# Performance work log

Hardware: AMD Instinct MI355X
Metric: run time of the kernel (lower is better)

The kernel has to match this reference:

```python
import jax, jax.numpy as jnp
import numpy as np

N, K, C, ECTX, HID = 4096, 48, 128, 384, 512
EPS = 1e-5
SCALE = 30.0

def _gelu(x):
    return jax.nn.gelu(x, approximate=False)

def _layernorm(x, g, b):
    mu = jnp.mean(x, axis=-1, keepdims=True)
    var = jnp.var(x, axis=-1, keepdims=True)
    return (x - mu) * jax.lax.rsqrt(var + EPS) * g + b

def setup_inputs() -> dict:
    key = jax.random.key(0)
    ks = jax.random.split(key, 12)
    d_in = C + ECTX  # 512
    def lin(k, out, inp):
        kw, kb = jax.random.split(k)
        lim = 1.0 / np.sqrt(inp)
        W = jax.random.uniform(kw, (out, inp), jnp.float32, -lim, lim)
        b = jax.random.uniform(kb, (out,), jnp.float32, -lim, lim)
        return W, b
    W_m1, b_m1 = lin(ks[0], C, d_in)   # message MLP: in->width
    W_m2, b_m2 = lin(ks[1], C, C)      # width->width
    W_m3, b_m3 = lin(ks[2], C, C)      # width->out
    W_d1, b_d1 = lin(ks[3], HID, C)    # dense MLP: in->hidden
    W_d2, b_d2 = lin(ks[4], C, HID)    # hidden->out
    return {
        "node_features": jax.random.normal(ks[5], (N, C), jnp.float32),
        "layer_edge_features": jax.random.normal(ks[6], (N, K, ECTX), jnp.float32),
        "mask": jnp.ones((N,), jnp.float32),
        "attention_mask": jnp.ones((N, K), jnp.float32),
        "W_m1": W_m1, "b_m1": b_m1, "W_m2": W_m2, "b_m2": b_m2,
        "W_m3": W_m3, "b_m3": b_m3,
        "g1": jnp.ones((C,), jnp.float32), "beta1": jnp.zeros((C,), jnp.float32),
        "W_d1": W_d1, "b_d1": b_d1, "W_d2": W_d2, "b_d2": b_d2,
        "g2": jnp.ones((C,), jnp.float32), "beta2": jnp.zeros((C,), jnp.float32),
    }

def reference(node_features, layer_edge_features, mask, attention_mask,
              W_m1, b_m1, W_m2, b_m2, W_m3, b_m3, g1, beta1,
              W_d1, b_d1, W_d2, b_d2, g2, beta2):
    # broadcast node features to every neighbor slot and concat edge context: (N, K, C+ECTX)
    h_exp = jnp.broadcast_to(node_features[:, None, :], (N, K, C))
    mlp_in = jnp.concatenate([h_exp, layer_edge_features], axis=-1)
    # per-edge message MLP (depth=2: two hidden gelu layers, linear out)
    h = _gelu(jnp.einsum("nkd,cd->nkc", mlp_in, W_m1) + b_m1)
    h = _gelu(jnp.einsum("nkc,dc->nkd", h, W_m2) + b_m2)
    message = jnp.einsum("nkc,dc->nkd", h, W_m3) + b_m3
    message = attention_mask[:, :, None] * message
    agg = jnp.sum(message, axis=-2) / SCALE            # (N, C)
    x = node_features + agg
    x = _layernorm(x, g1, beta1)
    # dense MLP (depth=1)
    d = _gelu(jnp.einsum("nc,hc->nh", x, W_d1) + b_d1)
    d = jnp.einsum("nh,ch->nc", d, W_d2) + b_d2
    x = x + d
    x = _layernorm(x, g2, beta2)
    return mask[:, None] * x
```

## Files before the change

kernel.cpp:

```cpp
#include <hip/hip_runtime.h>

#define NN 4096
#define KK 48
#define CC 128
#define EC 384
#define DD 512
#define HH 512

typedef short bf16x8 __attribute__((ext_vector_type(8)));
typedef float f32x4 __attribute__((ext_vector_type(4)));

__device__ __forceinline__ unsigned int pk2(float lo, float hi){
  unsigned int r;
  asm("v_cvt_pk_bf16_f32 %0, %1, %2" : "=v"(r) : "v"(lo), "v"(hi));
  return r;
}
__device__ __forceinline__ unsigned short f2bf(float x){
  return (unsigned short)pk2(x, x);
}
__device__ __forceinline__ bf16x8 pack8(f32x4 a, f32x4 b){
  union { unsigned int w[4]; bf16x8 v; } u;
  u.w[0]=pk2(a[0],a[1]); u.w[1]=pk2(a[2],a[3]);
  u.w[2]=pk2(b[0],b[1]); u.w[3]=pk2(b[2],b[3]);
  return u.v;
}

__device__ __forceinline__ float gelu_f(float x){
  float s = 1.5957691216057308f * (x + 0.044715f*x*x*x);
  float e = __expf(s);
  float t = 1.0f - 2.0f/(e + 1.0f);
  return 0.5f*x*(1.0f + t);
}

__global__ void cvt_kernel(const float* __restrict__ W1, const float* __restrict__ W2,
                           const float* __restrict__ W3, const float* __restrict__ Wd1,
                           const float* __restrict__ Wd2, unsigned short* __restrict__ o){
  int i = blockIdx.x*256 + threadIdx.x;
  float v;
  if      (i <  65536) v = W1[i];
  else if (i <  81920) v = W2[i-65536];
  else if (i <  98304) v = W3[i-81920];
  else if (i < 163840) v = Wd1[i-98304];
  else                 v = Wd2[i-163840];
  o[i] = f2bf(v);
}

__global__ __launch_bounds__(256, 4) void node_kernel(
    const float* __restrict__ nodef, const unsigned short* __restrict__ W1b,
    const float* __restrict__ b1, float* __restrict__ Y)
{
  const int tid  = threadIdx.x;
  const int lane = tid & 63;
  const int wid  = tid >> 6;
  const int l15  = lane & 15;
  const int lg   = lane >> 4;
  const int lg8  = lg*8;
  const int rowb = blockIdx.x*64 + wid*16;

  f32x4 acc[8];
  #pragma unroll
  for (int nt=0; nt<8; ++nt) acc[nt] = (f32x4){0.f,0.f,0.f,0.f};

  const float* arow = nodef + (size_t)(rowb + l15)*CC;
  #pragma unroll
  for (int ks=0; ks<4; ++ks){
    const int k0 = ks*32;
    bf16x8 af = pack8(*(const f32x4*)(arow + k0 + lg8), *(const f32x4*)(arow + k0 + lg8 + 4));
    #pragma unroll
    for (int nt=0; nt<8; ++nt){
      bf16x8 bf_ = *(const bf16x8*)(W1b + (size_t)(nt*16 + l15)*DD + k0 + lg8);
      acc[nt] = __builtin_amdgcn_mfma_f32_16x16x32_bf16(af, bf_, acc[nt], 0,0,0);
    }
  }
  #pragma unroll
  for (int nt=0; nt<8; ++nt){
    const int c = nt*16 + l15;
    const float bb = b1[c];
    #pragma unroll
    for (int j=0; j<4; ++j)
      Y[(size_t)(rowb + lg*4 + j)*CC + c] = acc[nt][j] + bb;
  }
}

__global__ __launch_bounds__(256, 4) void msg_kernel(
    const float* __restrict__ nodef, const float* __restrict__ edgef,
    const float* __restrict__ attn, const float* __restrict__ Y,
    const unsigned short* __restrict__ W1b,
    const unsigned short* __restrict__ W2b, const float* __restrict__ b2,
    const unsigned short* __restrict__ W3b, const float* __restrict__ b3,
    float* __restrict__ x1)
{
  __shared__ __attribute__((aligned(16))) unsigned short H[96][136];

  const int tid  = threadIdx.x;
  const int lane = tid & 63;
  const int wid  = tid >> 6;
  const int wm   = wid & 1;
  const int wn   = wid >> 1;
  const int l15  = lane & 15;
  const int lg   = lane >> 4;
  const int lg8  = lg*8;
  const int node = blockIdx.x*2 + wm;
  const int colb = wn*64;

  const float* erow[3];
  #pragma unroll
  for (int mt=0; mt<3; ++mt)
    erow[mt] = edgef + ((size_t)node*KK + (mt*16 + l15))*EC;

  float yv[4];
  #pragma unroll
  for (int nt=0; nt<4; ++nt)
    yv[nt] = Y[(size_t)node*CC + colb + nt*16 + l15];

  f32x4 acc[3][4];
  #pragma unroll
  for (int mt=0; mt<3; ++mt)
    #pragma unroll
    for (int nt=0; nt<4; ++nt)
      #pragma unroll
      for (int j=0; j<4; ++j) acc[mt][nt][j] = yv[nt];

  bf16x8 aC[3], bC[4], aN[3], bN[4];
  #pragma unroll
  for (int nt=0; nt<4; ++nt)
    bC[nt] = *(const bf16x8*)(W1b + (size_t)(colb + nt*16 + l15)*DD + CC + lg8);
  #pragma unroll
  for (int mt=0; mt<3; ++mt)
    aC[mt] = pack8(*(const f32x4*)(erow[mt] + lg8), *(const f32x4*)(erow[mt] + lg8 + 4));

  #pragma unroll
  for (int ks=0; ks<12; ++ks){
    if (ks < 11){
      const int k1 = (ks+1)*32;
      #pragma unroll
      for (int nt=0; nt<4; ++nt)
        bN[nt] = *(const bf16x8*)(W1b + (size_t)(colb + nt*16 + l15)*DD + CC + k1 + lg8);
      #pragma unroll
      for (int mt=0; mt<3; ++mt)
        aN[mt] = pack8(*(const f32x4*)(erow[mt] + k1 + lg8), *(const f32x4*)(erow[mt] + k1 + lg8 + 4));
    }
    #pragma unroll
    for (int mt=0; mt<3; ++mt)
      #pragma unroll
      for (int nt=0; nt<4; ++nt)
        acc[mt][nt] = __builtin_amdgcn_mfma_f32_16x16x32_bf16(aC[mt], bC[nt], acc[mt][nt], 0,0,0);
    #pragma unroll
    for (int mt=0; mt<3; ++mt) aC[mt] = aN[mt];
    #pragma unroll
    for (int nt=0; nt<4; ++nt) bC[nt] = bN[nt];
  }

  #pragma unroll
  for (int nt=0; nt<4; ++nt){
    const int c = colb + nt*16 + l15;
    #pragma unroll
    for (int mt=0; mt<3; ++mt){
      const int r0 = wm*48 + mt*16 + lg*4;
      #pragma unroll
      for (int j=0; j<4; ++j)
        H[r0+j][c] = f2bf(gelu_f(acc[mt][nt][j]));
    }
  }
  __syncthreads();

  f32x4 a2[3][4];
  #pragma unroll
  for (int mt=0; mt<3; ++mt)
    #pragma unroll
    for (int nt=0; nt<4; ++nt) a2[mt][nt] = (f32x4){0.f,0.f,0.f,0.f};

  #pragma unroll
  for (int ks=0; ks<4; ++ks){
    const int k0 = ks*32;
    bf16x8 bf_[4], af_[3];
    #pragma unroll
    for (int nt=0; nt<4; ++nt)
      bf_[nt] = *(const bf16x8*)(W2b + (size_t)(colb + nt*16 + l15)*CC + k0 + lg8);
    #pragma unroll
    for (int mt=0; mt<3; ++mt)
      af_[mt] = *(const bf16x8*)&H[wm*48 + mt*16 + l15][k0 + lg8];
    #pragma unroll
    for (int mt=0; mt<3; ++mt)
      #pragma unroll
      for (int nt=0; nt<4; ++nt)
        a2[mt][nt] = __builtin_amdgcn_mfma_f32_16x16x32_bf16(af_[mt], bf_[nt], a2[mt][nt], 0,0,0);
  }
  __syncthreads();

  #pragma unroll
  for (int nt=0; nt<4; ++nt){
    const int c = colb + nt*16 + l15;
    const float bb = b2[c];
    #pragma unroll
    for (int mt=0; mt<3; ++mt){
      const int r0 = wm*48 + mt*16 + lg*4;
      #pragma unroll
      for (int j=0; j<4; ++j)
        H[r0+j][c] = f2bf(gelu_f(a2[mt][nt][j] + bb));
    }
  }
  __syncthreads();

  f32x4 a3[3][4];
  #pragma unroll
  for (int mt=0; mt<3; ++mt)
    #pragma unroll
    for (int nt=0; nt<4; ++nt) a3[mt][nt] = (f32x4){0.f,0.f,0.f,0.f};

  #pragma unroll
  for (int ks=0; ks<4; ++ks){
    const int k0 = ks*32;
    bf16x8 bf_[4], af_[3];
    #pragma unroll
    for (int nt=0; nt<4; ++nt)
      bf_[nt] = *(const bf16x8*)(W3b + (size_t)(colb + nt*16 + l15)*CC + k0 + lg8);
    #pragma unroll
    for (int mt=0; mt<3; ++mt)
      af_[mt] = *(const bf16x8*)&H[wm*48 + mt*16 + l15][k0 + lg8];
    #pragma unroll
    for (int mt=0; mt<3; ++mt)
      #pragma unroll
      for (int nt=0; nt<4; ++nt)
        a3[mt][nt] = __builtin_amdgcn_mfma_f32_16x16x32_bf16(af_[mt], bf_[nt], a3[mt][nt], 0,0,0);
  }

  float av[3][4];
  #pragma unroll
  for (int mt=0; mt<3; ++mt)
    #pragma unroll
    for (int j=0; j<4; ++j)
      av[mt][j] = attn[(size_t)node*KK + mt*16 + lg*4 + j];

  #pragma unroll
  for (int nt=0; nt<4; ++nt){
    const int c = colb + nt*16 + l15;
    const float bb = b3[c];
    float t = 0.f;
    #pragma unroll
    for (int mt=0; mt<3; ++mt)
      #pragma unroll
      for (int j=0; j<4; ++j)
        t += (a3[mt][nt][j] + bb) * av[mt][j];
    t += __shfl_xor(t, 16, 64);
    t += __shfl_xor(t, 32, 64);
    if (lg == 0)
      x1[(size_t)node*CC + c] = nodef[(size_t)node*CC + c] + t*(1.0f/30.0f);
  }
}

__global__ __launch_bounds__(256, 2) void post_kernel(
    const float* __restrict__ x1, const float* __restrict__ mask,
    const float* __restrict__ g1, const float* __restrict__ be1,
    const unsigned short* __restrict__ Wd1b, const float* __restrict__ bd1,
    const unsigned short* __restrict__ Wd2b, const float* __restrict__ bd2,
    const float* __restrict__ g2, const float* __restrict__ be2,
    float* __restrict__ out)
{
  __shared__ __attribute__((aligned(16))) unsigned short xlnB[16][136];
  __shared__ __attribute__((aligned(16))) float          xlnF[16][132];
  __shared__ __attribute__((aligned(16))) unsigned short Hb[16][520];
  __shared__ __attribute__((aligned(16))) float          x2s[16][132];

  const int tid  = threadIdx.x;
  const int lane = tid & 63;
  const int wid  = tid >> 6;
  const int l15  = lane & 15;
  const int lg   = lane >> 4;
  const int lg8  = lg*8;
  const int n0   = blockIdx.x * 16;

  {
    const int nl = tid >> 4;
    const int s  = tid & 15;
    const float* row = x1 + (size_t)(n0+nl)*CC + s*8;
    f32x4 a = *(const f32x4*)row;
    f32x4 b = *(const f32x4*)(row+4);
    float sm = (a[0]+a[1])+(a[2]+a[3]) + (b[0]+b[1])+(b[2]+b[3]);
    float sq = a[0]*a[0]+a[1]*a[1]+a[2]*a[2]+a[3]*a[3]
             + b[0]*b[0]+b[1]*b[1]+b[2]*b[2]+b[3]*b[3];
    sm += __shfl_xor(sm,1,64); sq += __shfl_xor(sq,1,64);
    sm += __shfl_xor(sm,2,64); sq += __shfl_xor(sq,2,64);
    sm += __shfl_xor(sm,4,64); sq += __shfl_xor(sq,4,64);
    sm += __shfl_xor(sm,8,64); sq += __shfl_xor(sq,8,64);
    const float mu = sm*(1.f/128.f);
    const float rs = rsqrtf(sq*(1.f/128.f) - mu*mu + 1e-5f);
    #pragma unroll
    for (int j=0; j<8; ++j){
      const int c = s*8+j;
      float xv = (j<4) ? a[j] : b[j-4];
      float y = (xv-mu)*rs*g1[c] + be1[c];
      xlnF[nl][c] = y;
      xlnB[nl][c] = f2bf(y);
    }
  }
  __syncthreads();

  f32x4 a1[8];
  #pragma unroll
  for (int nt=0; nt<8; ++nt) a1[nt] = (f32x4){0.f,0.f,0.f,0.f};
  #pragma unroll
  for (int ks=0; ks<4; ++ks){
    const int k0 = ks*32;
    bf16x8 af = *(const bf16x8*)&xlnB[l15][k0 + lg8];
    #pragma unroll
    for (int nt=0; nt<8; ++nt){
      const int h = wid*128 + nt*16 + l15;
      bf16x8 bf_ = *(const bf16x8*)(Wd1b + (size_t)h*CC + k0 + lg8);
      a1[nt] = __builtin_amdgcn_mfma_f32_16x16x32_bf16(af, bf_, a1[nt], 0,0,0);
    }
  }
  #pragma unroll
  for (int nt=0; nt<8; ++nt){
    const int h = wid*128 + nt*16 + l15;
    const float bb = bd1[h];
    #pragma unroll
    for (int j=0; j<4; ++j)
      Hb[lg*4+j][h] = f2bf(gelu_f(a1[nt][j] + bb));
  }
  __syncthreads();

  f32x4 a2[2];
  #pragma unroll
  for (int nt=0; nt<2; ++nt) a2[nt] = (f32x4){0.f,0.f,0.f,0.f};
  #pragma unroll
  for (int ks=0; ks<16; ++ks){
    const int k0 = ks*32;
    bf16x8 af = *(const bf16x8*)&Hb[l15][k0 + lg8];
    #pragma unroll
    for (int nt=0; nt<2; ++nt){
      const int c = wid*32 + nt*16 + l15;
      bf16x8 bf_ = *(const bf16x8*)(Wd2b + (size_t)c*HH + k0 + lg8);
      a2[nt] = __builtin_amdgcn_mfma_f32_16x16x32_bf16(af, bf_, a2[nt], 0,0,0);
    }
  }
  #pragma unroll
  for (int nt=0; nt<2; ++nt){
    const int c = wid*32 + nt*16 + l15;
    const float bb = bd2[c];
    #pragma unroll
    for (int j=0; j<4; ++j){
      const int r = lg*4 + j;
      x2s[r][c] = xlnF[r][c] + a2[nt][j] + bb;
    }
  }
  __syncthreads();

  {
    const int nl = tid >> 4;
    const int s  = tid & 15;
    float xv[8];
    float sm = 0.f, sq = 0.f;
    #pragma unroll
    for (int j=0; j<8; ++j){ xv[j] = x2s[nl][s*8+j]; sm += xv[j]; sq += xv[j]*xv[j]; }
    sm += __shfl_xor(sm,1,64); sq += __shfl_xor(sq,1,64);
    sm += __shfl_xor(sm,2,64); sq += __shfl_xor(sq,2,64);
    sm += __shfl_xor(sm,4,64); sq += __shfl_xor(sq,4,64);
    sm += __shfl_xor(sm,8,64); sq += __shfl_xor(sq,8,64);
    const float mu = sm*(1.f/128.f);
    const float rs = rsqrtf(sq*(1.f/128.f) - mu*mu + 1e-5f);
    const float mk = mask[n0+nl];
    f32x4 o0, o1;
    #pragma unroll
    for (int j=0; j<8; ++j){
      const int c = s*8+j;
      float y = (xv[j]-mu)*rs*g2[c] + be2[c];
      if (j < 4) o0[j] = mk*y; else o1[j-4] = mk*y;
    }
    float* orow = out + (size_t)(n0+nl)*CC + s*8;
    *(f32x4*)orow     = o0;
    *(f32x4*)(orow+4) = o1;
  }
}

extern "C" void kernel_launch(void* const* d_in, const int* in_sizes, int n_in,
                              void* d_out, int out_size, void* d_ws, size_t ws_size,
                              hipStream_t stream)
{
  (void)in_sizes; (void)n_in; (void)out_size; (void)ws_size;

  const float* nodef = (const float*)d_in[0];
  const float* edgef = (const float*)d_in[1];
  const float* mask  = (const float*)d_in[2];
  const float* attn  = (const float*)d_in[3];
  const float* W_m1  = (const float*)d_in[4];
  const float* b_m1  = (const float*)d_in[5];
  const float* W_m2  = (const float*)d_in[6];
  const float* b_m2  = (const float*)d_in[7];
  const float* W_m3  = (const float*)d_in[8];
  const float* b_m3  = (const float*)d_in[9];
  const float* g1    = (const float*)d_in[10];
  const float* be1   = (const float*)d_in[11];
  const float* W_d1  = (const float*)d_in[12];
  const float* b_d1  = (const float*)d_in[13];
  const float* W_d2  = (const float*)d_in[14];
  const float* b_d2  = (const float*)d_in[15];
  const float* g2    = (const float*)d_in[16];
  const float* be2   = (const float*)d_in[17];

  unsigned short* wsb  = (unsigned short*)d_ws;
  unsigned short* W1b  = wsb;
  unsigned short* W2b  = wsb + 65536;
  unsigned short* W3b  = wsb + 81920;
  unsigned short* Wd1b = wsb + 98304;
  unsigned short* Wd2b = wsb + 163840;
  float* x1 = (float*)((char*)d_ws + 458752);
  float* Y  = (float*)((char*)d_ws + 2555904);

  cvt_kernel<<<896, 256, 0, stream>>>(W_m1, W_m2, W_m3, W_d1, W_d2, wsb);
  node_kernel<<<64, 256, 0, stream>>>(nodef, W1b, b_m1, Y);
  msg_kernel<<<2048, 256, 0, stream>>>(nodef, edgef, attn, Y,
                                       W1b, W2b, b_m2, W3b, b_m3, x1);
  post_kernel<<<256, 256, 0, stream>>>(x1, mask, g1, be1, Wd1b, b_d1,
                                       Wd2b, b_d2, g2, be2, (float*)d_out);
}
```

Measured before the change: 544.9 us.

## Fuse post-MLP into message kernel and stage edge features via async LDS DMA

Edge-feature tiles for the first message layer now go through a triple-buffered LDS ring filled by global_load_lds with an XOR swizzle, instead of direct per-lane global loads. The post kernel (layernorm, dense MLP, layernorm, mask) is folded into the tail of msg_kernel, so the x1 round trip and one launch go away. Occupancy drops from 4 to 2 blocks per SM because of the larger LDS footprint. The fused dense MLP uses only 2 of 16 MFMA rows per block, which wastes matrix throughput and re-reads the dense weights once per block.

```diff
diff --git a/kernel.cpp b/kernel.cpp
--- a/kernel.cpp
+++ b/kernel.cpp
@@ -9,27 +9,27 @@
 
 typedef short bf16x8 __attribute__((ext_vector_type(8)));
 typedef float f32x4 __attribute__((ext_vector_type(4)));
-
-__device__ __forceinline__ unsigned int pk2(float lo, float hi){
-  unsigned int r;
-  asm("v_cvt_pk_bf16_f32 %0, %1, %2" : "=v"(r) : "v"(lo), "v"(hi));
-  return r;
-}
-__device__ __forceinline__ unsigned short f2bf(float x){
-  return (unsigned short)pk2(x, x);
-}
+typedef unsigned int u32;
+
+typedef const __attribute__((address_space(1))) void* gas1_t;
+typedef __attribute__((address_space(3))) void* las3_t;
+
+#define CB() asm volatile("" ::: "memory")
+
+__device__ __forceinline__ u32 pk2(float lo, float hi){
+  u32 r; asm("v_cvt_pk_bf16_f32 %0, %1, %2" : "=v"(r) : "v"(lo), "v"(hi)); return r;
+}
+__device__ __forceinline__ unsigned short f2bf(float x){ return (unsigned short)pk2(x,x); }
 __device__ __forceinline__ bf16x8 pack8(f32x4 a, f32x4 b){
-  union { unsigned int w[4]; bf16x8 v; } u;
+  union { u32 w[4]; bf16x8 v; } u;
   u.w[0]=pk2(a[0],a[1]); u.w[1]=pk2(a[2],a[3]);
   u.w[2]=pk2(b[0],b[1]); u.w[3]=pk2(b[2],b[3]);
   return u.v;
 }
-
 __device__ __forceinline__ float gelu_f(float x){
-  float s = 1.5957691216057308f * (x + 0.044715f*x*x*x);
+  float s = 1.5957691216057308f*(x + 0.044715f*x*x*x);
   float e = __expf(s);
-  float t = 1.0f - 2.0f/(e + 1.0f);
-  return 0.5f*x*(1.0f + t);
+  return 0.5f*x*(1.f + (1.f - 2.f/(e+1.f)));
 }
 
 __global__ void cvt_kernel(const float* __restrict__ W1, const float* __restrict__ W2,
@@ -82,15 +82,27 @@
   }
 }
 
-__global__ __launch_bounds__(256, 4) void msg_kernel(
+__global__ __launch_bounds__(256, 2) void msg_kernel(
     const float* __restrict__ nodef, const float* __restrict__ edgef,
     const float* __restrict__ attn, const float* __restrict__ Y,
     const unsigned short* __restrict__ W1b,
     const unsigned short* __restrict__ W2b, const float* __restrict__ b2,
     const unsigned short* __restrict__ W3b, const float* __restrict__ b3,
-    float* __restrict__ x1)
+    const float* __restrict__ g1v, const float* __restrict__ be1,
+    const unsigned short* __restrict__ Wd1b, const float* __restrict__ bd1,
+    const unsigned short* __restrict__ Wd2b, const float* __restrict__ bd2,
+    const float* __restrict__ g2v, const float* __restrict__ be2,
+    const float* __restrict__ maskv, float* __restrict__ out)
 {
+  __shared__ __attribute__((aligned(16))) char SA[36864];
   __shared__ __attribute__((aligned(16))) unsigned short H[96][136];
+
+  float (*Abuf)[96*32] = (float(*)[96*32])SA;
+  unsigned short (*xlnB)[136] = (unsigned short(*)[136])SA;
+  float* xlnF = (float*)(SA + 4352);
+  float* x1s  = (float*)(SA + 5376);
+  unsigned short (*Hd)[520] = (unsigned short(*)[520])(SA + 6400);
+  float* x2s  = (float*)(SA + 23040);
 
   const int tid  = threadIdx.x;
   const int lane = tid & 63;
@@ -100,13 +112,28 @@
   const int l15  = lane & 15;
   const int lg   = lane >> 4;
   const int lg8  = lg*8;
-  const int node = blockIdx.x*2 + wm;
-  const int colb = wn*64;
-
-  const float* erow[3];
-  #pragma unroll
-  for (int mt=0; mt<3; ++mt)
-    erow[mt] = edgef + ((size_t)node*KK + (mt*16 + l15))*EC;
+  const int node0 = blockIdx.x*2;
+  const int node  = node0 + wm;
+  const int colb  = wn*64;
+
+  const float* gsrc = edgef + (size_t)node0*KK*EC;
+  int dma_r[3], dma_s4[3];
+  #pragma unroll
+  for (int i=0;i<3;++i){
+    int c = wid*3 + i;
+    int r = c*8 + (lane>>3);
+    int s = (lane&7) ^ (r&7);
+    dma_r[i] = r;
+    dma_s4[i] = s*4;
+  }
+
+#define STAGE(B_, T_)                                                              \
+  { _Pragma("unroll")                                                              \
+    for (int i_=0;i_<3;++i_){                                                      \
+      __builtin_amdgcn_global_load_lds(                                            \
+        (gas1_t)(gsrc + (size_t)dma_r[i_]*EC + (T_)*32 + dma_s4[i_]),              \
+        (las3_t)&Abuf[B_][(wid*3+i_)*256], 16, 0, 0);                              \
+    } }
 
   float yv[4];
   #pragma unroll
@@ -121,32 +148,45 @@
       #pragma unroll
       for (int j=0; j<4; ++j) acc[mt][nt][j] = yv[nt];
 
-  bf16x8 aC[3], bC[4], aN[3], bN[4];
+  CB();
+  bf16x8 bC[4], bN[4];
   #pragma unroll
   for (int nt=0; nt<4; ++nt)
     bC[nt] = *(const bf16x8*)(W1b + (size_t)(colb + nt*16 + l15)*DD + CC + lg8);
-  #pragma unroll
-  for (int mt=0; mt<3; ++mt)
-    aC[mt] = pack8(*(const f32x4*)(erow[mt] + lg8), *(const f32x4*)(erow[mt] + lg8 + 4));
-
-  #pragma unroll
-  for (int ks=0; ks<12; ++ks){
-    if (ks < 11){
-      const int k1 = (ks+1)*32;
+  CB();
+  STAGE(0, 0); CB();
+  STAGE(1, 1); CB();
+
+  #pragma unroll
+  for (int t=0; t<12; ++t){
+    const int cur = t % 3;
+    if (t < 11){
       #pragma unroll
       for (int nt=0; nt<4; ++nt)
-        bN[nt] = *(const bf16x8*)(W1b + (size_t)(colb + nt*16 + l15)*DD + CC + k1 + lg8);
-      #pragma unroll
-      for (int mt=0; mt<3; ++mt)
-        aN[mt] = pack8(*(const f32x4*)(erow[mt] + k1 + lg8), *(const f32x4*)(erow[mt] + k1 + lg8 + 4));
+        bN[nt] = *(const bf16x8*)(W1b + (size_t)(colb + nt*16 + l15)*DD + CC + (t+1)*32 + lg8);
+    }
+    CB();
+    if (t < 11) asm volatile("s_waitcnt vmcnt(7)" ::: "memory");
+    else        asm volatile("s_waitcnt vmcnt(0)" ::: "memory");
+    __builtin_amdgcn_s_barrier();
+    CB();
+    if (t+2 < 12){ STAGE((t+2)%3, t+2); }
+    CB();
+    bf16x8 a_[3];
+    #pragma unroll
+    for (int mt=0; mt<3; ++mt){
+      const int r  = wm*48 + mt*16 + l15;
+      const int s0 = (2*lg)   ^ (r&7);
+      const int s1 = (2*lg+1) ^ (r&7);
+      f32x4 lo = *(const f32x4*)&Abuf[cur][r*32 + s0*4];
+      f32x4 hi = *(const f32x4*)&Abuf[cur][r*32 + s1*4];
+      a_[mt] = pack8(lo, hi);
     }
     #pragma unroll
     for (int mt=0; mt<3; ++mt)
       #pragma unroll
       for (int nt=0; nt<4; ++nt)
-        acc[mt][nt] = __builtin_amdgcn_mfma_f32_16x16x32_bf16(aC[mt], bC[nt], acc[mt][nt], 0,0,0);
-    #pragma unroll
-    for (int mt=0; mt<3; ++mt) aC[mt] = aN[mt];
+        acc[mt][nt] = __builtin_amdgcn_mfma_f32_16x16x32_bf16(a_[mt], bC[nt], acc[mt][nt], 0,0,0);
     #pragma unroll
     for (int nt=0; nt<4; ++nt) bC[nt] = bN[nt];
   }
@@ -232,6 +272,7 @@
     for (int j=0; j<4; ++j)
       av[mt][j] = attn[(size_t)node*KK + mt*16 + lg*4 + j];
 
+  float tt[4];
   #pragma unroll
   for (int nt=0; nt<4; ++nt){
     const int c = colb + nt*16 + l15;
@@ -244,61 +285,37 @@
         t += (a3[mt][nt][j] + bb) * av[mt][j];
     t += __shfl_xor(t, 16, 64);
     t += __shfl_xor(t, 32, 64);
-    if (lg == 0)
-      x1[(size_t)node*CC + c] = nodef[(size_t)node*CC + c] + t*(1.0f/30.0f);
-  }
-}
-
-__global__ __launch_bounds__(256, 2) void post_kernel(
-    const float* __restrict__ x1, const float* __restrict__ mask,
-    const float* __restrict__ g1, const float* __restrict__ be1,
-    const unsigned short* __restrict__ Wd1b, const float* __restrict__ bd1,
-    const unsigned short* __restrict__ Wd2b, const float* __restrict__ bd2,
-    const float* __restrict__ g2, const float* __restrict__ be2,
-    float* __restrict__ out)
-{
-  __shared__ __attribute__((aligned(16))) unsigned short xlnB[16][136];
-  __shared__ __attribute__((aligned(16))) float          xlnF[16][132];
-  __shared__ __attribute__((aligned(16))) unsigned short Hb[16][520];
-  __shared__ __attribute__((aligned(16))) float          x2s[16][132];
-
-  const int tid  = threadIdx.x;
-  const int lane = tid & 63;
-  const int wid  = tid >> 6;
-  const int l15  = lane & 15;
-  const int lg   = lane >> 4;
-  const int lg8  = lg*8;
-  const int n0   = blockIdx.x * 16;
-
-  {
-    const int nl = tid >> 4;
-    const int s  = tid & 15;
-    const float* row = x1 + (size_t)(n0+nl)*CC + s*8;
-    f32x4 a = *(const f32x4*)row;
-    f32x4 b = *(const f32x4*)(row+4);
-    float sm = (a[0]+a[1])+(a[2]+a[3]) + (b[0]+b[1])+(b[2]+b[3]);
-    float sq = a[0]*a[0]+a[1]*a[1]+a[2]*a[2]+a[3]*a[3]
-             + b[0]*b[0]+b[1]*b[1]+b[2]*b[2]+b[3]*b[3];
-    sm += __shfl_xor(sm,1,64); sq += __shfl_xor(sq,1,64);
-    sm += __shfl_xor(sm,2,64); sq += __shfl_xor(sq,2,64);
-    sm += __shfl_xor(sm,4,64); sq += __shfl_xor(sq,4,64);
-    sm += __shfl_xor(sm,8,64); sq += __shfl_xor(sq,8,64);
+    tt[nt] = t;
+  }
+  if (lg == 0){
+    #pragma unroll
+    for (int nt=0; nt<4; ++nt){
+      const int c = colb + nt*16 + l15;
+      x1s[wm*128 + c] = nodef[(size_t)node*CC + c] + tt[nt]*(1.0f/30.0f);
+    }
+  }
+  __syncthreads();
+
+  if (wid < 2){
+    float v0 = x1s[wid*128 + lane];
+    float v1 = x1s[wid*128 + 64 + lane];
+    float sm = v0+v1, sq = v0*v0+v1*v1;
+    #pragma unroll
+    for (int d=1; d<64; d<<=1){ sm += __shfl_xor(sm,d,64); sq += __shfl_xor(sq,d,64); }
     const float mu = sm*(1.f/128.f);
     const float rs = rsqrtf(sq*(1.f/128.f) - mu*mu + 1e-5f);
-    #pragma unroll
-    for (int j=0; j<8; ++j){
-      const int c = s*8+j;
-      float xv = (j<4) ? a[j] : b[j-4];
-      float y = (xv-mu)*rs*g1[c] + be1[c];
-      xlnF[nl][c] = y;
-      xlnB[nl][c] = f2bf(y);
-    }
-  }
-  __syncthreads();
-
-  f32x4 a1[8];
-  #pragma unroll
-  for (int nt=0; nt<8; ++nt) a1[nt] = (f32x4){0.f,0.f,0.f,0.f};
+    float y0 = (v0-mu)*rs*g1v[lane]    + be1[lane];
+    float y1 = (v1-mu)*rs*g1v[lane+64] + be1[lane+64];
+    xlnF[wid*128 + lane]      = y0;
+    xlnF[wid*128 + 64 + lane] = y1;
+    xlnB[wid][lane]      = f2bf(y0);
+    xlnB[wid][lane + 64] = f2bf(y1);
+  }
+  __syncthreads();
+
+  f32x4 d1acc[8];
+  #pragma unroll
+  for (int nt=0; nt<8; ++nt) d1acc[nt] = (f32x4){0.f,0.f,0.f,0.f};
   #pragma unroll
   for (int ks=0; ks<4; ++ks){
     const int k0 = ks*32;
@@ -307,70 +324,59 @@
     for (int nt=0; nt<8; ++nt){
       const int h = wid*128 + nt*16 + l15;
       bf16x8 bf_ = *(const bf16x8*)(Wd1b + (size_t)h*CC + k0 + lg8);
-      a1[nt] = __builtin_amdgcn_mfma_f32_16x16x32_bf16(af, bf_, a1[nt], 0,0,0);
-    }
-  }
-  #pragma unroll
-  for (int nt=0; nt<8; ++nt){
-    const int h = wid*128 + nt*16 + l15;
-    const float bb = bd1[h];
-    #pragma unroll
-    for (int j=0; j<4; ++j)
-      Hb[lg*4+j][h] = f2bf(gelu_f(a1[nt][j] + bb));
-  }
-  __syncthreads();
-
-  f32x4 a2[2];
-  #pragma unroll
-  for (int nt=0; nt<2; ++nt) a2[nt] = (f32x4){0.f,0.f,0.f,0.f};
+      d1acc[nt] = __builtin_amdgcn_mfma_f32_16x16x32_bf16(af, bf_, d1acc[nt], 0,0,0);
+    }
+  }
+  if (lg == 0){
+    #pragma unroll
+    for (int nt=0; nt<8; ++nt){
+      const int h = wid*128 + nt*16 + l15;
+      const float bb = bd1[h];
+      Hd[0][h] = f2bf(gelu_f(d1acc[nt][0] + bb));
+      Hd[1][h] = f2bf(gelu_f(d1acc[nt][1] + bb));
+    }
+  }
+  __syncthreads();
+
+  f32x4 d2acc[2];
+  #pragma unroll
+  for (int nt=0; nt<2; ++nt) d2acc[nt] = (f32x4){0.f,0.f,0.f,0.f};
   #pragma unroll
   for (int ks=0; ks<16; ++ks){
     const int k0 = ks*32;
-    bf16x8 af = *(const bf16x8*)&Hb[l15][k0 + lg8];
+    bf16x8 af = *(const bf16x8*)&Hd[l15][k0 + lg8];
     #pragma unroll
     for (int nt=0; nt<2; ++nt){
       const int c = wid*32 + nt*16 + l15;
       bf16x8 bf_ = *(const bf16x8*)(Wd2b + (size_t)c*HH + k0 + lg8);
-      a2[nt] = __builtin_amdgcn_mfma_f32_16x16x32_bf16(af, bf_, a2[nt], 0,0,0);
-    }
-  }
-  #pragma unroll
-  for (int nt=0; nt<2; ++nt){
-    const int c = wid*32 + nt*16 + l15;
-    const float bb = bd2[c];
-    #pragma unroll
-    for (int j=0; j<4; ++j){
-      const int r = lg*4 + j;
-      x2s[r][c] = xlnF[r][c] + a2[nt][j] + bb;
-    }
-  }
-  __syncthreads();
-
-  {
-    const int nl = tid >> 4;
-    const int s  = tid & 15;
-    float xv[8];
-    float sm = 0.f, sq = 0.f;
-    #pragma unroll
-    for (int j=0; j<8; ++j){ xv[j] = x2s[nl][s*8+j]; sm += xv[j]; sq += xv[j]*xv[j]; }
-    sm += __shfl_xor(sm,1,64); sq += __shfl_xor(sq,1,64);
-    sm += __shfl_xor(sm,2,64); sq += __shfl_xor(sq,2,64);
-    sm += __shfl_xor(sm,4,64); sq += __shfl_xor(sq,4,64);
-    sm += __shfl_xor(sm,8,64); sq += __shfl_xor(sq,8,64);
+      d2acc[nt] = __builtin_amdgcn_mfma_f32_16x16x32_bf16(af, bf_, d2acc[nt], 0,0,0);
+    }
+  }
+  if (lg == 0){
+    #pragma unroll
+    for (int nt=0; nt<2; ++nt){
+      const int c = wid*32 + nt*16 + l15;
+      const float bb = bd2[c];
+      x2s[0*128 + c] = xlnF[0*128 + c] + d2acc[nt][0] + bb;
+      x2s[1*128 + c] = xlnF[1*128 + c] + d2acc[nt][1] + bb;
+    }
+  }
+  __syncthreads();
+
+  if (wid < 2){
+    const int gn = node0 + wid;
+    float v0 = x2s[wid*128 + lane];
+    float v1 = x2s[wid*128 + 64 + lane];
+    float sm = v0+v1, sq = v0*v0+v1*v1;
+    #pragma unroll
+    for (int d=1; d<64; d<<=1){ sm += __shfl_xor(sm,d,64); sq += __shfl_xor(sq,d,64); }
     const float mu = sm*(1.f/128.f);
     const float rs = rsqrtf(sq*(1.f/128.f) - mu*mu + 1e-5f);
-    const float mk = mask[n0+nl];
-    f32x4 o0, o1;
-    #pragma unroll
-    for (int j=0; j<8; ++j){
-      const int c = s*8+j;
-      float y = (xv[j]-mu)*rs*g2[c] + be2[c];
-      if (j < 4) o0[j] = mk*y; else o1[j-4] = mk*y;
-    }
-    float* orow = out + (size_t)(n0+nl)*CC + s*8;
-    *(f32x4*)orow     = o0;
-    *(f32x4*)(orow+4) = o1;
-  }
+    const float mk = maskv[gn];
+    out[(size_t)gn*CC + lane]      = mk*((v0-mu)*rs*g2v[lane]    + be2[lane]);
+    out[(size_t)gn*CC + 64 + lane] = mk*((v1-mu)*rs*g2v[lane+64] + be2[lane+64]);
+  }
+#undef STAGE
 }
 
 extern "C" void kernel_launch(void* const* d_in, const int* in_sizes, int n_in,
@@ -404,13 +410,12 @@
   unsigned short* W3b  = wsb + 81920;
   unsigned short* Wd1b = wsb + 98304;
   unsigned short* Wd2b = wsb + 163840;
-  float* x1 = (float*)((char*)d_ws + 458752);
-  float* Y  = (float*)((char*)d_ws + 2555904);
+  float* Y = (float*)((char*)d_ws + 458752);
 
   cvt_kernel<<<896, 256, 0, stream>>>(W_m1, W_m2, W_m3, W_d1, W_d2, wsb);
   node_kernel<<<64, 256, 0, stream>>>(nodef, W1b, b_m1, Y);
   msg_kernel<<<2048, 256, 0, stream>>>(nodef, edgef, attn, Y,
-                                       W1b, W2b, b_m2, W3b, b_m3, x1);
-  post_kernel<<<256, 256, 0, stream>>>(x1, mask, g1, be1, Wd1b, b_d1,
-                                       Wd2b, b_d2, g2, be2, (float*)d_out);
-}
+                                       W1b, W2b, b_m2, W3b, b_m3,
+                                       g1, be1, Wd1b, b_d1, Wd2b, b_d2,
+                                       g2, be2, mask, (float*)d_out);
+}
```

Result: no change. 548.4 us (+0.7%).
